# Performance work log

Measured on AMD Instinct MI355X. Metric: run time of the kernel, lower is better.

Reference implementation:

```python
import jax, jax.numpy as jnp
import numpy as np

N = 2048
FEAT = 64

def setup_inputs() -> dict:
    key = jax.random.key(0)
    ks = jax.random.split(key, 9)
    s = lambda fan_in: 1.0 / np.sqrt(fan_in)
    return {
        "asset_features": jax.random.normal(ks[0], (N, FEAT), jnp.float32),
        "Wp": jax.random.uniform(ks[1], (32, FEAT), jnp.float32, -s(FEAT), s(FEAT)),
        "bp": jax.random.uniform(ks[2], (32,), jnp.float32, -s(FEAT), s(FEAT)),
        "W1": jax.random.uniform(ks[3], (32, 64), jnp.float32, -s(64), s(64)),
        "b1": jax.random.uniform(ks[4], (32,), jnp.float32, -s(64), s(64)),
        "W2": jax.random.uniform(ks[5], (16, 32), jnp.float32, -s(32), s(32)),
        "b2": jax.random.uniform(ks[6], (16,), jnp.float32, -s(32), s(32)),
        "W3": jax.random.uniform(ks[7], (1, 16), jnp.float32, -s(16), s(16)),
        "b3": jax.random.uniform(ks[8], (1,), jnp.float32, -s(16), s(16)),
    }

def reference(asset_features, Wp, bp, W1, b1, W2, b2, W3, b3):
    n = asset_features.shape[0]
    # projected: [N, 32]
    proj = asset_features @ Wp.T + bp
    # First similarity layer acts on concat([proj_i, proj_j]) of size 64.
    # Split W1 into the halves acting on i-features and j-features so we
    # never materialize the [N, N, 64] concat tensor.
    Wa, Wb = W1[:, :32], W1[:, 32:]
    pa = proj @ Wa.T            # [N, 32] contribution of row asset i
    pb = proj @ Wb.T            # [N, 32] contribution of col asset j
    h1 = jax.nn.relu(pa[:, None, :] + pb[None, :, :] + b1)   # [N, N, 32]
    h2 = jax.nn.relu(jnp.einsum('ijk,hk->ijh', h1, W2) + b2)  # [N, N, 16]
    sim = jax.nn.sigmoid(jnp.einsum('ijh,h->ij', h2, W3[0]) + b3[0])  # [N, N]
    # Diagonal forced to 1.0, matching fill_diagonal_(1.0)
    eye = jnp.eye(n, dtype=bool)
    return jnp.where(eye, jnp.float32(1.0), sim)
```

## Files before the change

kernel.cpp:

```cpp
#include <hip/hip_runtime.h>
#include <hip/hip_fp16.h>

#define NN 2048

typedef _Float16 f16x8 __attribute__((ext_vector_type(8)));
typedef float f32x4 __attribute__((ext_vector_type(4)));

__global__ __launch_bounds__(256) void prep_kernel(
    const float* __restrict__ A, const float* __restrict__ Wp,
    const float* __restrict__ bp, const float* __restrict__ W1,
    const float* __restrict__ b1,
    _Float16* __restrict__ pa, _Float16* __restrict__ pb)
{
    __shared__ float projLDS[8][32];
    const int t = threadIdx.x;
    const int rl = t >> 5;
    const int k  = t & 31;
    const int row = blockIdx.x * 8 + rl;

    const float4* xa = (const float4*)(A + row * 64);
    const float4* wp = (const float4*)(Wp + k * 64);
    float acc = bp[k];
#pragma unroll
    for (int m = 0; m < 16; ++m) {
        float4 xv = xa[m], wv = wp[m];
        acc += xv.x * wv.x + xv.y * wv.y + xv.z * wv.z + xv.w * wv.w;
    }
    projLDS[rl][k] = acc;
    __syncthreads();

    const float4* w1a = (const float4*)(W1 + k * 64);
    const float4* w1b = (const float4*)(W1 + k * 64 + 32);
    const float4* pr  = (const float4*)(projLDS[rl]);
    float sa = b1[k], sb = 0.f;
#pragma unroll
    for (int m = 0; m < 8; ++m) {
        float4 p = pr[m], wa = w1a[m], wb = w1b[m];
        sa += p.x * wa.x + p.y * wa.y + p.z * wa.z + p.w * wa.w;
        sb += p.x * wb.x + p.y * wb.y + p.z * wb.z + p.w * wb.w;
    }
    pa[row * 32 + k] = (_Float16)sa;
    pb[row * 32 + k] = (_Float16)sb;
}

__global__ __launch_bounds__(256, 8) void sim_kernel(
    const _Float16* __restrict__ pa, const _Float16* __restrict__ pb,
    const float* __restrict__ W2, const float* __restrict__ b2,
    const float* __restrict__ W3, const float* __restrict__ b3,
    float* __restrict__ out)
{
    __shared__ _Float16 paLDS[32 * 32];
    const int t    = threadIdx.x;
    const int lane = t & 63;
    const int wid  = t >> 6;
    const int i0 = (blockIdx.x >> 5) * 32;
    const int jb = (((blockIdx.x & 31) << 2) + wid) * 16;
    const int n  = lane & 15;
    const int q  = lane >> 4;

    ((uint2*)paLDS)[t] = ((const uint2*)(pa + (size_t)i0 * 32))[t];

    const f16x8 pbf = *(const f16x8*)(pb + (size_t)(jb + n) * 32 + q * 8);

    f16x8 w2f;
    {
        const float* w2r = W2 + n * 32 + q * 8;
#pragma unroll
        for (int e = 0; e < 8; ++e) w2f[e] = (_Float16)w2r[e];
    }

    f32x4 cinit;
    float w3r[4];
#pragma unroll
    for (int r = 0; r < 4; ++r) {
        cinit[r] = b2[q * 4 + r];
        w3r[r]   = W3[q * 4 + r];
    }
    const float b3v = b3[0];
    const f16x8 zero = {};

    __syncthreads();

    float* outp = out + (size_t)(i0 + q) * NN + jb + n;

#pragma unroll 2
    for (int tt = 0; tt < 8; ++tt) {
        float s0, s1, s2, s3;
#pragma unroll
        for (int r4 = 0; r4 < 4; ++r4) {
            const int ii = 4 * tt + r4;
            f16x8 af = *(const f16x8*)&paLDS[ii * 32 + q * 8];
            f16x8 h1 = __builtin_elementwise_max(af + pbf, zero);
            f32x4 d = __builtin_amdgcn_mfma_f32_16x16x32_f16(w2f, h1, cinit, 0, 0, 0);
            float p = 0.f;
#pragma unroll
            for (int r = 0; r < 4; ++r)
                p = fmaf(fmaxf(d[r], 0.f), w3r[r], p);
            p += __shfl_xor(p, 16, 64);
            p += __shfl_xor(p, 32, 64);
            if (r4 == 0) s0 = p; else if (r4 == 1) s1 = p;
            else if (r4 == 2) s2 = p; else s3 = p;
        }
        const float z = (q < 2 ? (q == 0 ? s0 : s1) : (q == 2 ? s2 : s3)) + b3v;
        float sim = __builtin_amdgcn_rcpf(1.f + __expf(-z));
        const int iMine = i0 + 4 * tt + q;
        if (iMine == jb + n) sim = 1.f;
        outp[(size_t)(4 * tt) * NN] = sim;
    }
}

extern "C" void kernel_launch(void* const* d_in, const int* in_sizes, int n_in,
                              void* d_out, int out_size, void* d_ws, size_t ws_size,
                              hipStream_t stream)
{
    const float* A  = (const float*)d_in[0];
    const float* Wp = (const float*)d_in[1];
    const float* bp = (const float*)d_in[2];
    const float* W1 = (const float*)d_in[3];
    const float* b1 = (const float*)d_in[4];
    const float* W2 = (const float*)d_in[5];
    const float* b2 = (const float*)d_in[6];
    const float* W3 = (const float*)d_in[7];
    const float* b3 = (const float*)d_in[8];
    float* out = (float*)d_out;

    _Float16* pa = (_Float16*)d_ws;
    _Float16* pb = pa + NN * 32;

    prep_kernel<<<NN / 8, 256, 0, stream>>>(A, Wp, bp, W1, b1, pa, pb);
    sim_kernel<<<2048, 256, 0, stream>>>(pa, pb, W2, b2, W3, b3, out);
}
```

Measured before the change: 94.31 us.

## Compute final W3 reduction with MFMA instead of cross-lane shuffles

The final 16-to-1 projection with W3 is now done by a second MFMA. The ReLU'd layer-2 outputs of row pairs are packed into fp16 pairs, and a parity-masked W3 fragment is multiplied against them, replacing the per-row FMA chain and two xor-shuffles. The four row MFMAs per iteration are also issued back to back to improve instruction-level parallelism. The trade-off is that layer-2 activations are rounded to fp16 (round-toward-zero) before the last dot product, which adds precision loss, and the lane/row mapping of the packed operand is intricate.

```diff
diff --git a/kernel.cpp b/kernel.cpp
--- a/kernel.cpp
+++ b/kernel.cpp
@@ -4,6 +4,7 @@
 #define NN 2048
 
 typedef _Float16 f16x8 __attribute__((ext_vector_type(8)));
+typedef _Float16 f16x2 __attribute__((ext_vector_type(2)));
 typedef float f32x4 __attribute__((ext_vector_type(4)));
 
 __global__ __launch_bounds__(256) void prep_kernel(
@@ -70,41 +71,60 @@
     }
 
     f32x4 cinit;
-    float w3r[4];
 #pragma unroll
-    for (int r = 0; r < 4; ++r) {
-        cinit[r] = b2[q * 4 + r];
-        w3r[r]   = W3[q * 4 + r];
-    }
+    for (int r = 0; r < 4; ++r) cinit[r] = b2[q * 4 + r];
+
+    f16x8 w3a;
+#pragma unroll
+    for (int e = 0; e < 8; ++e)
+        w3a[e] = ((e & 1) == (n & 1)) ? (_Float16)W3[q * 4 + (e >> 1)]
+                                      : (_Float16)0.f;
+
     const float b3v = b3[0];
+    f32x4 cinit2;
+#pragma unroll
+    for (int r = 0; r < 4; ++r) cinit2[r] = b3v;
+
     const f16x8 zero = {};
 
     __syncthreads();
 
     float* outp = out + (size_t)(i0 + q) * NN + jb + n;
 
+    union B2U { f16x8 v; f16x2 p[4]; };
+
 #pragma unroll 2
     for (int tt = 0; tt < 8; ++tt) {
-        float s0, s1, s2, s3;
+        const _Float16* base = &paLDS[(4 * tt) * 32 + q * 8];
+        f16x8 a0 = *(const f16x8*)(base);
+        f16x8 a1 = *(const f16x8*)(base + 32);
+        f16x8 a2 = *(const f16x8*)(base + 64);
+        f16x8 a3 = *(const f16x8*)(base + 96);
+        f16x8 h0 = __builtin_elementwise_max(a0 + pbf, zero);
+        f16x8 h1 = __builtin_elementwise_max(a1 + pbf, zero);
+        f16x8 h2 = __builtin_elementwise_max(a2 + pbf, zero);
+        f16x8 h3 = __builtin_elementwise_max(a3 + pbf, zero);
+
+        f32x4 d0 = __builtin_amdgcn_mfma_f32_16x16x32_f16(w2f, h0, cinit, 0, 0, 0);
+        f32x4 d1 = __builtin_amdgcn_mfma_f32_16x16x32_f16(w2f, h1, cinit, 0, 0, 0);
+        f32x4 d2 = __builtin_amdgcn_mfma_f32_16x16x32_f16(w2f, h2, cinit, 0, 0, 0);
+        f32x4 d3 = __builtin_amdgcn_mfma_f32_16x16x32_f16(w2f, h3, cinit, 0, 0, 0);
+
+        B2U pk01, pk23;
 #pragma unroll
-        for (int r4 = 0; r4 < 4; ++r4) {
-            const int ii = 4 * tt + r4;
-            f16x8 af = *(const f16x8*)&paLDS[ii * 32 + q * 8];
-            f16x8 h1 = __builtin_elementwise_max(af + pbf, zero);
-            f32x4 d = __builtin_amdgcn_mfma_f32_16x16x32_f16(w2f, h1, cinit, 0, 0, 0);
-            float p = 0.f;
-#pragma unroll
-            for (int r = 0; r < 4; ++r)
-                p = fmaf(fmaxf(d[r], 0.f), w3r[r], p);
-            p += __shfl_xor(p, 16, 64);
-            p += __shfl_xor(p, 32, 64);
-            if (r4 == 0) s0 = p; else if (r4 == 1) s1 = p;
-            else if (r4 == 2) s2 = p; else s3 = p;
+        for (int r = 0; r < 4; ++r) {
+            pk01.p[r] = __builtin_bit_cast(f16x2,
+                __builtin_amdgcn_cvt_pkrtz(fmaxf(d0[r], 0.f), fmaxf(d1[r], 0.f)));
+            pk23.p[r] = __builtin_bit_cast(f16x2,
+                __builtin_amdgcn_cvt_pkrtz(fmaxf(d2[r], 0.f), fmaxf(d3[r], 0.f)));
         }
-        const float z = (q < 2 ? (q == 0 ? s0 : s1) : (q == 2 ? s2 : s3)) + b3v;
+        f32x4 l01 = __builtin_amdgcn_mfma_f32_16x16x32_f16(w3a, pk01.v, cinit2, 0, 0, 0);
+        f32x4 l23 = __builtin_amdgcn_mfma_f32_16x16x32_f16(w3a, pk23.v, cinit2, 0, 0, 0);
+
+        const float z = q == 0 ? l01[0] : q == 1 ? l01[1]
+                      : q == 2 ? l23[0] : l23[1];
         float sim = __builtin_amdgcn_rcpf(1.f + __expf(-z));
-        const int iMine = i0 + 4 * tt + q;
-        if (iMine == jb + n) sim = 1.f;
+        if (i0 + 4 * tt + q == jb + n) sim = 1.f;
         outp[(size_t)(4 * tt) * NN] = sim;
     }
 }
```

After: 96.23 us (median of 2 runs). +2.0%, slower.
